# Optimization experiments

Hardware: AMD Instinct MI355X
Metric: run time of the kernel (lower is better)

Reference implementation:

```python
import jax, jax.numpy as jnp
import numpy as np

B, N, PAST = 2, 1024, 1024
DIM, HEADS, DH = 2048, 16, 128
INNER = HEADS * DH
LN_EPS = 1e-5
ROPE_THETA = 10000.0


def setup_inputs() -> dict:
    key = jax.random.key(0)
    k0, k1, k2, k3, k4 = jax.random.split(key, 5)
    x = jax.random.normal(k0, (B, N, DIM), dtype=jnp.float32)
    past_k = jax.random.normal(k1, (B, HEADS, PAST, DH), dtype=jnp.float32)
    past_v = jax.random.normal(k2, (B, HEADS, PAST, DH), dtype=jnp.float32)
    # causal mask with KV-cache offset: query i sits at global pos PAST+i,
    # mask (True = blocked) keys at positions j > PAST+i
    kv = PAST + N
    q_pos = PAST + jnp.arange(N)
    k_pos = jnp.arange(kv)
    mask = jnp.broadcast_to((k_pos[None, :] > q_pos[:, None])[None, None], (B, 1, N, kv))
    w_qkv = jax.random.normal(k3, (DIM, 3 * INNER), dtype=jnp.float32) * (DIM ** -0.5)
    w_out = jax.random.normal(k4, (INNER, DIM), dtype=jnp.float32) * (INNER ** -0.5)
    ln_g = jnp.ones((DIM,), dtype=jnp.float32)
    ln_b = jnp.zeros((DIM,), dtype=jnp.float32)
    return {"x": x, "past_k": past_k, "past_v": past_v, "mask": mask,
            "w_qkv": w_qkv, "w_out": w_out, "ln_g": ln_g, "ln_b": ln_b}


def _layernorm(x, g, b):
    mu = jnp.mean(x, axis=-1, keepdims=True)
    var = jnp.mean((x - mu) ** 2, axis=-1, keepdims=True)
    return (x - mu) * jax.lax.rsqrt(var + LN_EPS) * g + b


def _rope(t, pos):
    # interleaved rotary (lucidrains rotary-embedding-torch convention)
    inv_freq = 1.0 / (ROPE_THETA ** (jnp.arange(0, DH, 2, dtype=jnp.float32) / DH))
    freqs = pos.astype(jnp.float32)[:, None] * inv_freq[None, :]   # [n, DH/2]
    freqs = jnp.repeat(freqs, 2, axis=-1)                          # [n, DH]
    cos = jnp.cos(freqs).astype(t.dtype)
    sin = jnp.sin(freqs).astype(t.dtype)
    t2 = t.reshape(*t.shape[:-1], DH // 2, 2)
    rot = jnp.stack((-t2[..., 1], t2[..., 0]), axis=-1).reshape(t.shape)
    return t * cos + rot * sin


def reference(x, past_k, past_v, mask, w_qkv, w_out, ln_g, ln_b):
    b, n, _ = x.shape
    xn = _layernorm(x, ln_g, ln_b)
    qkv = xn @ w_qkv                                               # [b, n, 3*INNER]
    q, k, v = jnp.split(qkv, 3, axis=-1)
    to_heads = lambda t: t.reshape(b, n, HEADS, DH).transpose(0, 2, 1, 3)  # b h n d
    q, k, v = to_heads(q), to_heads(k), to_heads(v)
    k = jnp.concatenate((past_k, k), axis=2)                       # [b, h, kv, d]
    v = jnp.concatenate((past_v, v), axis=2)
    kv_len = k.shape[2]
    q = _rope(q, jnp.arange(n) + (kv_len - n))
    k = _rope(k, jnp.arange(kv_len))
    scale = DH ** -0.5
    dots = jnp.einsum('bhnd,bhmd->bhnm', q, k) * scale             # [b, h, n, kv]
    dots = jnp.where(mask, -jnp.inf, dots)
    attn = jax.nn.softmax(dots, axis=-1)
    out = jnp.einsum('bhnm,bhmd->bhnd', attn, v)                   # [b, h, n, d]
    out = out.transpose(0, 2, 1, 3).reshape(b, n, INNER)
    return out @ w_out, k, v
```

## Files before the change

kernel.cpp:

```cpp
#include <hip/hip_runtime.h>
#include <hip/hip_bf16.h>
#include <math.h>

#define BB    2
#define NN    1024
#define PAST  1024
#define KVL   2048
#define DIM   2048
#define HEADS 16
#define DH    128
#define INNER 2048
#define NQKV  6144
#define TOK   2048
#define LN_EPS 1e-5f

typedef __attribute__((ext_vector_type(8))) short   short8;
typedef __attribute__((ext_vector_type(4))) float   f32x4;
typedef __attribute__((ext_vector_type(8))) unsigned short us8;
typedef __attribute__((ext_vector_type(4))) unsigned short us4;
typedef unsigned short us;

__device__ __forceinline__ float bfbits2f(us u) {
    return __uint_as_float(((unsigned int)u) << 16);
}
__device__ __forceinline__ us f2bfb(float f) {
    union { __hip_bfloat16 h; us u; } cv;
    cv.h = __float2bfloat16(f);
    return cv.u;
}
__device__ __forceinline__ us8 pack8u(float4 a, float4 b) {
    us8 r;
    r[0] = f2bfb(a.x); r[1] = f2bfb(a.y); r[2] = f2bfb(a.z); r[3] = f2bfb(a.w);
    r[4] = f2bfb(b.x); r[5] = f2bfb(b.y); r[6] = f2bfb(b.z); r[7] = f2bfb(b.w);
    return r;
}

__device__ __forceinline__ void gload_lds16(const void* gsrc, void* ldst) {
    __builtin_amdgcn_global_load_lds(
        (const __attribute__((address_space(1))) void*)gsrc,
        (__attribute__((address_space(3))) void*)ldst, 16, 0, 0);
}

__global__ __launch_bounds__(256) void transp_kernel(
    const float* __restrict__ src, us* __restrict__ dst, int R, int C)
{
    const int c0 = blockIdx.x * 64;
    const int r0 = blockIdx.y * 64;
    const int tid = threadIdx.x;

    __shared__ us T[64][68];

    #pragma unroll
    for (int e = 0; e < 4; e++) {
        int idx = tid + e * 256;
        int jr  = idx >> 4;
        int c4  = (idx & 15) * 4;
        float4 v = *reinterpret_cast<const float4*>(
            src + (size_t)(r0 + jr) * C + c0 + c4);
        us4 w;
        w[0] = f2bfb(v.x); w[1] = f2bfb(v.y); w[2] = f2bfb(v.z); w[3] = f2bfb(v.w);
        *reinterpret_cast<us4*>(&T[jr][c4]) = w;
    }
    __syncthreads();

    #pragma unroll
    for (int e = 0; e < 4; e++) {
        int idx = tid + e * 256;
        int d   = idx >> 4;
        int k4  = (idx & 15) * 4;
        us4 w;
        w[0] = T[k4 + 0][d];
        w[1] = T[k4 + 1][d];
        w[2] = T[k4 + 2][d];
        w[3] = T[k4 + 3][d];
        *reinterpret_cast<us4*>(dst + (size_t)(c0 + d) * R + r0 + k4) = w;
    }
}

__global__ __launch_bounds__(256) void ln_kernel(
    const float* __restrict__ x, const float* __restrict__ g,
    const float* __restrict__ b, us* __restrict__ xn)
{
    const int t   = blockIdx.x;
    const int tid = threadIdx.x;
    const size_t base = (size_t)t * DIM;

    float4 p0 = reinterpret_cast<const float4*>(x + base)[tid * 2 + 0];
    float4 p1 = reinterpret_cast<const float4*>(x + base)[tid * 2 + 1];
    float v[8] = {p0.x, p0.y, p0.z, p0.w, p1.x, p1.y, p1.z, p1.w};

    float s1 = 0.f, s2 = 0.f;
    #pragma unroll
    for (int i = 0; i < 8; i++) { s1 += v[i]; s2 += v[i] * v[i]; }

    #pragma unroll
    for (int off = 32; off; off >>= 1) {
        s1 += __shfl_xor(s1, off);
        s2 += __shfl_xor(s2, off);
    }
    __shared__ float red1[4], red2[4];
    if ((tid & 63) == 0) { red1[tid >> 6] = s1; red2[tid >> 6] = s2; }
    __syncthreads();
    float S1 = red1[0] + red1[1] + red1[2] + red1[3];
    float S2 = red2[0] + red2[1] + red2[2] + red2[3];
    const float inv = 1.0f / (float)DIM;
    float mu  = S1 * inv;
    float var = S2 * inv - mu * mu;
    float rstd = rsqrtf(var + LN_EPS);

    const int d0 = tid * 8;
    float4 oa, ob;
    oa.x = (v[0] - mu) * rstd * g[d0 + 0] + b[d0 + 0];
    oa.y = (v[1] - mu) * rstd * g[d0 + 1] + b[d0 + 1];
    oa.z = (v[2] - mu) * rstd * g[d0 + 2] + b[d0 + 2];
    oa.w = (v[3] - mu) * rstd * g[d0 + 3] + b[d0 + 3];
    ob.x = (v[4] - mu) * rstd * g[d0 + 4] + b[d0 + 4];
    ob.y = (v[5] - mu) * rstd * g[d0 + 5] + b[d0 + 5];
    ob.z = (v[6] - mu) * rstd * g[d0 + 6] + b[d0 + 6];
    ob.w = (v[7] - mu) * rstd * g[d0 + 7] + b[d0 + 7];

    *reinterpret_cast<us8*>(xn + base + d0) = pack8u(oa, ob);
}

template<bool OUT_BF16>
__global__ __launch_bounds__(256) void gemm_bt_kernel(
    const us* __restrict__ A, const us* __restrict__ Bt,
    void* __restrict__ Cout, int M, int N, int K)
{
    __shared__ us As[2][128 * 32];
    __shared__ us Bs[2][128 * 32];

    const int tid  = threadIdx.x;
    const int wave = tid >> 6, lane = tid & 63;
    const int quad = lane >> 4, l16 = lane & 15;
    const int wm = wave & 1, wn = wave >> 1;
    const int m0 = blockIdx.y * 128, n0 = blockIdx.x * 128;

    f32x4 acc[4][4];
    #pragma unroll
    for (int i = 0; i < 4; i++)
        #pragma unroll
        for (int j = 0; j < 4; j++)
            #pragma unroll
            for (int r = 0; r < 4; r++) acc[i][j][r] = 0.f;

    const int s_row = tid >> 2;
    const int s_c8  = (tid & 3) * 8;

    auto stage = [&](int k0, int buf) {
        #pragma unroll
        for (int e = 0; e < 2; e++) {
            gload_lds16(A  + (size_t)(m0 + e * 64 + s_row) * K + k0 + s_c8,
                        (char*)&As[buf][0] + (e * 256 + tid) * 16);
            gload_lds16(Bt + (size_t)(n0 + e * 64 + s_row) * K + k0 + s_c8,
                        (char*)&Bs[buf][0] + (e * 256 + tid) * 16);
        }
    };

    stage(0, 0);
    __syncthreads();

    int buf = 0;
    for (int k0 = 0; k0 < K; k0 += 32) {
        if (k0 + 32 < K) stage(k0 + 32, buf ^ 1);

        short8 af[4], bf[4];
        #pragma unroll
        for (int mi = 0; mi < 4; mi++)
            af[mi] = *reinterpret_cast<const short8*>(
                &As[buf][(wm * 64 + mi * 16 + l16) * 32 + quad * 8]);
        #pragma unroll
        for (int ni = 0; ni < 4; ni++)
            bf[ni] = *reinterpret_cast<const short8*>(
                &Bs[buf][(wn * 64 + ni * 16 + l16) * 32 + quad * 8]);

        __builtin_amdgcn_s_setprio(1);
        #pragma unroll
        for (int mi = 0; mi < 4; mi++)
            #pragma unroll
            for (int ni = 0; ni < 4; ni++)
                acc[mi][ni] = __builtin_amdgcn_mfma_f32_16x16x32_bf16(
                    af[mi], bf[ni], acc[mi][ni], 0, 0, 0);
        __builtin_amdgcn_s_setprio(0);

        __syncthreads();
        buf ^= 1;
    }

    #pragma unroll
    for (int mi = 0; mi < 4; mi++) {
        #pragma unroll
        for (int r = 0; r < 4; r++) {
            size_t row = (size_t)(m0 + wm * 64 + mi * 16 + quad * 4 + r);
            #pragma unroll
            for (int ni = 0; ni < 4; ni++) {
                size_t col = n0 + wn * 64 + ni * 16 + l16;
                if (OUT_BF16)
                    ((us*)Cout)[row * N + col] = f2bfb(acc[mi][ni][r]);
                else
                    ((float*)Cout)[row * N + col] = acc[mi][ni][r];
            }
        }
    }
}

__global__ __launch_bounds__(256) void rope_kernel(
    const float* __restrict__ past_k, const float* __restrict__ past_v,
    us* __restrict__ qkv, float* __restrict__ out_k, float* __restrict__ out_v,
    us* __restrict__ Kbf)
{
    const int tid  = threadIdx.x;
    const int pid  = blockIdx.x * 4 + (tid >> 6);
    const int lane = tid & 63;

    const int b   = pid / (HEADS * KVL);
    const int rem = pid - b * (HEADS * KVL);
    const int h   = rem / KVL;
    const int pos = rem - h * KVL;

    const float invf = exp2f((float)lane * (-13.287712379549449f / 64.0f));
    float sn, cs;
    sincosf((float)pos * invf, &sn, &cs);

    const size_t obase = ((size_t)(b * HEADS + h) * KVL + pos) * DH + 2 * lane;

    float k0, k1;
    if (pos < PAST) {
        const size_t pbase = ((size_t)(b * HEADS + h) * PAST + pos) * DH + 2 * lane;
        k0 = past_k[pbase];
        k1 = past_k[pbase + 1];
    } else {
        const int t = b * NN + (pos - PAST);
        const us* qp = qkv + (size_t)t * NQKV + INNER + h * DH + 2 * lane;
        k0 = bfbits2f(qp[0]); k1 = bfbits2f(qp[1]);
    }
    float kr0 = k0 * cs - k1 * sn;
    float kr1 = k1 * cs + k0 * sn;
    out_k[obase]     = kr0;
    out_k[obase + 1] = kr1;
    Kbf[obase]       = f2bfb(kr0);
    Kbf[obase + 1]   = f2bfb(kr1);

    if (pos < PAST) {
        const size_t pbase = ((size_t)(b * HEADS + h) * PAST + pos) * DH + 2 * lane;
        out_v[obase]     = past_v[pbase];
        out_v[obase + 1] = past_v[pbase + 1];
    } else {
        const int t = b * NN + (pos - PAST);
        const us* vp = qkv + (size_t)t * NQKV + 2 * INNER + h * DH + 2 * lane;
        out_v[obase]     = bfbits2f(vp[0]);
        out_v[obase + 1] = bfbits2f(vp[1]);
    }

    if (pos >= PAST) {
        const int t = b * NN + (pos - PAST);
        us* qq = qkv + (size_t)t * NQKV + h * DH + 2 * lane;
        float q0 = bfbits2f(qq[0]), q1 = bfbits2f(qq[1]);
        qq[0] = f2bfb(q0 * cs - q1 * sn);
        qq[1] = f2bfb(q1 * cs + q0 * sn);
    }
}

__global__ __launch_bounds__(256) void vtrans_kernel(
    const float* __restrict__ Vc, us* __restrict__ Vtg)
{
    const int jb = blockIdx.x;
    const int db = blockIdx.y;
    const int bh = blockIdx.z;
    const int tid = threadIdx.x;

    __shared__ us T[64][68];

    const float* src = Vc + ((size_t)bh * KVL + jb * 64) * DH + db * 64;
    #pragma unroll
    for (int e = 0; e < 4; e++) {
        int idx = tid + e * 256;
        int jr  = idx >> 4;
        int c4  = (idx & 15) * 4;
        float4 v = *reinterpret_cast<const float4*>(src + (size_t)jr * DH + c4);
        us4 w;
        w[0] = f2bfb(v.x); w[1] = f2bfb(v.y); w[2] = f2bfb(v.z); w[3] = f2bfb(v.w);
        *reinterpret_cast<us4*>(&T[jr][c4]) = w;
    }
    __syncthreads();

    us* dst = Vtg + ((size_t)bh * DH + db * 64) * KVL + jb * 64;
    #pragma unroll
    for (int e = 0; e < 4; e++) {
        int idx = tid + e * 256;
        int d   = idx >> 4;
        int k4  = (idx & 15) * 4;
        us4 w;
        w[0] = T[k4 + 0][d];
        w[1] = T[k4 + 1][d];
        w[2] = T[k4 + 2][d];
        w[3] = T[k4 + 3][d];
        *reinterpret_cast<us4*>(dst + (size_t)d * KVL + k4) = w;
    }
}

__global__ __launch_bounds__(256) void attn_mfma_kernel(
    const us* __restrict__ qkv,
    const us* __restrict__ Kbf,
    const us* __restrict__ Vtg,
    us* __restrict__ Ao)
{
    const int qt   = blockIdx.x;
    const int h    = blockIdx.y;
    const int b    = blockIdx.z;
    const int tid  = threadIdx.x;
    const int wave = tid >> 6;
    const int lane = tid & 63;
    const int quad = lane >> 4;
    const int l16  = lane & 15;

    __shared__ us Ks[2][64 * 128];
    __shared__ us Vt[2][128 * 64];
    __shared__ us Pb[64][72];
    __shared__ float alF[4][16];

    short8 qf[4];
    {
        const int qrow = qt * 64 + wave * 16 + l16;
        const us* qp = qkv + (size_t)(b * NN + qrow) * NQKV + h * DH;
        #pragma unroll
        for (int ks = 0; ks < 4; ks++)
            qf[ks] = *reinterpret_cast<const short8*>(qp + ks * 32 + quad * 8);
    }

    f32x4 Oacc[8];
    #pragma unroll
    for (int t = 0; t < 8; t++)
        #pragma unroll
        for (int r = 0; r < 4; r++) Oacc[t][r] = 0.f;
    float m_run  = -INFINITY;
    float l_part = 0.f;

    const us* kptr = Kbf + (size_t)(b * HEADS + h) * KVL * DH;
    const us* vtb  = Vtg + (size_t)(b * HEADS + h) * DH * KVL;
    const float scale = 0.08838834764831845f;
    const float THRU  = 90.50966799f;
    const int qg  = PAST + qt * 64 + wave * 16 + l16;
    const int nch = 17 + qt;

    auto stage = [&](int j0, int buf) {
        #pragma unroll
        for (int e = 0; e < 4; e++) {
            int phys = (e * 256 + tid) * 16;
            int row  = phys >> 8;
            int col  = (phys & 255) ^ ((row & 7) << 4);
            gload_lds16((const char*)(kptr + (size_t)(j0 + row) * DH) + col,
                        (char*)&Ks[buf][0] + phys);
        }
        #pragma unroll
        for (int e = 0; e < 4; e++) {
            int phys = (e * 256 + tid) * 16;
            int row  = phys >> 7;
            int col  = (phys & 127) ^ ((row & 7) << 4);
            gload_lds16((const char*)(vtb + (size_t)row * KVL + j0) + col,
                        (char*)&Vt[buf][0] + phys);
        }
    };

    stage(0, 0);
    __syncthreads();

    int cur = 0;
    for (int c = 0; c < nch; c++) {
        const int j0 = c * 64;
        if (c + 1 < nch) stage(j0 + 64, cur ^ 1);

        f32x4 S[4];
        #pragma unroll
        for (int t = 0; t < 4; t++)
            #pragma unroll
            for (int r = 0; r < 4; r++) S[t][r] = 0.f;
        __builtin_amdgcn_s_setprio(1);
        #pragma unroll
        for (int ks = 0; ks < 4; ks++) {
            #pragma unroll
            for (int t = 0; t < 4; t++) {
                int row  = t * 16 + l16;
                int colb = ks * 64 + quad * 16;
                const char* p = (const char*)&Ks[cur][0] +
                                row * 256 + (colb ^ ((row & 7) << 4));
                short8 kb = *reinterpret_cast<const short8*>(p);
                S[t] = __builtin_amdgcn_mfma_f32_16x16x32_bf16(kb, qf[ks], S[t], 0, 0, 0);
            }
        }
        __builtin_amdgcn_s_setprio(0);

        const int rel = qg - j0;
        float mx = -INFINITY;
        #pragma unroll
        for (int t = 0; t < 4; t++) {
            #pragma unroll
            for (int r = 0; r < 4; r++) {
                int koff = t * 16 + quad * 4 + r;
                S[t][r] = (koff <= rel) ? S[t][r] : -INFINITY;
                mx = fmaxf(mx, S[t][r]);
            }
        }
        mx = fmaxf(mx, __shfl_xor(mx, 16));
        mx = fmaxf(mx, __shfl_xor(mx, 32));

        float alpha = 1.f;
        if (__any(mx > m_run + THRU)) {
            float nm = fmaxf(m_run, mx);
            alpha = __expf((m_run - nm) * scale);
            m_run = nm;
            if (quad == 0) alF[wave][l16] = alpha;
            asm volatile("s_waitcnt lgkmcnt(0)" ::: "memory");
            float a0 = alF[wave][quad * 4 + 0];
            float a1 = alF[wave][quad * 4 + 1];
            float a2 = alF[wave][quad * 4 + 2];
            float a3 = alF[wave][quad * 4 + 3];
            #pragma unroll
            for (int t2 = 0; t2 < 8; t2++) {
                Oacc[t2][0] *= a0; Oacc[t2][1] *= a1;
                Oacc[t2][2] *= a2; Oacc[t2][3] *= a3;
            }
        }

        const float nmk = -m_run * scale;
        float rs = 0.f;
        #pragma unroll
        for (int t = 0; t < 4; t++) {
            us4 w;
            #pragma unroll
            for (int r = 0; r < 4; r++) {
                float p = __expf(fmaf(S[t][r], scale, nmk));
                rs += p;
                w[r] = f2bfb(p);
            }
            *reinterpret_cast<us4*>(&Pb[wave * 16 + l16][t * 16 + quad * 4]) = w;
        }
        l_part = l_part * alpha + rs;

        asm volatile("s_waitcnt lgkmcnt(0)" ::: "memory");
        __builtin_amdgcn_sched_barrier(0);

        __builtin_amdgcn_s_setprio(1);
        #pragma unroll
        for (int kh = 0; kh < 2; kh++) {
            short8 pa = *reinterpret_cast<const short8*>(
                &Pb[wave * 16 + l16][kh * 32 + quad * 8]);
            #pragma unroll
            for (int t2 = 0; t2 < 8; t2++) {
                int row  = t2 * 16 + l16;
                int colb = kh * 64 + quad * 16;
                const char* p = (const char*)&Vt[cur][0] +
                                row * 128 + (colb ^ ((row & 7) << 4));
                short8 vb = *reinterpret_cast<const short8*>(p);
                Oacc[t2] = __builtin_amdgcn_mfma_f32_16x16x32_bf16(pa, vb, Oacc[t2], 0, 0, 0);
            }
        }
        __builtin_amdgcn_s_setprio(0);

        __syncthreads();
        cur ^= 1;
    }

    l_part += __shfl_xor(l_part, 16);
    l_part += __shfl_xor(l_part, 32);
    float invl[4];
    #pragma unroll
    for (int r = 0; r < 4; r++)
        invl[r] = 1.f / __shfl(l_part, quad * 4 + r);

    const int row0 = b * NN + qt * 64 + wave * 16 + quad * 4;
    #pragma unroll
    for (int r = 0; r < 4; r++) {
        us* dst = Ao + (size_t)(row0 + r) * INNER + h * DH + l16;
        #pragma unroll
        for (int t2 = 0; t2 < 8; t2++)
            dst[t2 * 16] = f2bfb(Oacc[t2][r] * invl[r]);
    }
}

extern "C" void kernel_launch(void* const* d_in, const int* in_sizes, int n_in,
                              void* d_out, int out_size, void* d_ws, size_t ws_size,
                              hipStream_t stream)
{
    const float* x      = (const float*)d_in[0];
    const float* past_k = (const float*)d_in[1];
    const float* past_v = (const float*)d_in[2];
    const float* w_qkv  = (const float*)d_in[4];
    const float* w_out  = (const float*)d_in[5];
    const float* ln_g   = (const float*)d_in[6];
    const float* ln_b   = (const float*)d_in[7];

    float* out   = (float*)d_out;
    float* out_k = out   + (size_t)BB * NN * DIM;
    float* out_v = out_k + (size_t)BB * HEADS * KVL * DH;

    us* xn   = (us*)d_ws;
    us* qkv  = xn  + (size_t)TOK * DIM;
    us* Wqt  = qkv + (size_t)TOK * NQKV;
    us* Wot  = Wqt + (size_t)NQKV * DIM;
    us* Vtg  = Wot + (size_t)DIM * INNER;
    us* attn = xn;
    us* Kbf  = Wqt;

    transp_kernel<<<dim3(NQKV / 64, DIM / 64), 256, 0, stream>>>(
        w_qkv, Wqt, DIM, NQKV);
    transp_kernel<<<dim3(DIM / 64, INNER / 64), 256, 0, stream>>>(
        w_out, Wot, INNER, DIM);

    ln_kernel<<<TOK, 256, 0, stream>>>(x, ln_g, ln_b, xn);

    gemm_bt_kernel<true><<<dim3(NQKV / 128, TOK / 128), 256, 0, stream>>>(
        xn, Wqt, (void*)qkv, TOK, NQKV, DIM);

    rope_kernel<<<(BB * HEADS * KVL) / 4, 256, 0, stream>>>(
        past_k, past_v, qkv, out_k, out_v, Kbf);

    vtrans_kernel<<<dim3(KVL / 64, DH / 64, BB * HEADS), 256, 0, stream>>>(
        out_v, Vtg);

    attn_mfma_kernel<<<dim3(NN / 64, HEADS, BB), 256, 0, stream>>>(
        qkv, Kbf, Vtg, attn);

    gemm_bt_kernel<false><<<dim3(DIM / 128, TOK / 128), 256, 0, stream>>>(
        attn, Wot, (void*)out, TOK, DIM, INNER);
}
```

Before: 381.3 us.

## Pair complementary causal query tiles per 512-thread attention block to balance work

The attention kernel now launches 256 blocks of 512 threads. Each block pairs query tile p with tile 15-p, so both halves share the same K/V staging and every block does a near-equal number of chunks, which removes the causal load imbalance. The flat block index is remapped so that neighbouring blocks cover different heads and batches. Alpha broadcast now uses shuffles instead of an LDS round-trip, and the per-wave P buffer is XOR-swizzled. The risk is idle waves in the low tile during the extra chunks, and lower occupancy from the larger blocks.

Measured after the change: 378.7 us. No clear change (-0.7%).

```diff
diff --git a/kernel.cpp b/kernel.cpp
--- a/kernel.cpp
+++ b/kernel.cpp
@@ -299,29 +299,35 @@
     }
 }
 
-__global__ __launch_bounds__(256) void attn_mfma_kernel(
+__global__ __launch_bounds__(512) void attn_mfma_kernel(
     const us* __restrict__ qkv,
     const us* __restrict__ Kbf,
     const us* __restrict__ Vtg,
     us* __restrict__ Ao)
 {
-    const int qt   = blockIdx.x;
-    const int h    = blockIdx.y;
-    const int b    = blockIdx.z;
     const int tid  = threadIdx.x;
     const int wave = tid >> 6;
     const int lane = tid & 63;
     const int quad = lane >> 4;
     const int l16  = lane & 15;
 
+    const int flat = blockIdx.x;
+    const int s    = flat >> 3;
+    const int g    = (flat & 7) + 8 * (s & 3);
+    const int p    = s >> 2;
+    const int h    = g & 15;
+    const int b    = g >> 4;
+    const int qtile = (wave < 4) ? p : (15 - p);
+    const int nch   = 32 - p;
+    const int mynch = (wave < 4) ? (17 + p) : (32 - p);
+
     __shared__ us Ks[2][64 * 128];
     __shared__ us Vt[2][128 * 64];
-    __shared__ us Pb[64][72];
-    __shared__ float alF[4][16];
+    __shared__ us Pb[8][16 * 64];
 
     short8 qf[4];
     {
-        const int qrow = qt * 64 + wave * 16 + l16;
+        const int qrow = qtile * 64 + (wave & 3) * 16 + l16;
         const us* qp = qkv + (size_t)(b * NN + qrow) * NQKV + h * DH;
         #pragma unroll
         for (int ks = 0; ks < 4; ks++)
@@ -340,24 +346,25 @@
     const us* vtb  = Vtg + (size_t)(b * HEADS + h) * DH * KVL;
     const float scale = 0.08838834764831845f;
     const float THRU  = 90.50966799f;
-    const int qg  = PAST + qt * 64 + wave * 16 + l16;
-    const int nch = 17 + qt;
+    const int qg  = PAST + qtile * 64 + (wave & 3) * 16 + l16;
+    const int swz = (l16 & 7) << 4;
+    char* pbb = (char*)&Pb[wave][0];
 
     auto stage = [&](int j0, int buf) {
         #pragma unroll
-        for (int e = 0; e < 4; e++) {
-            int phys = (e * 256 + tid) * 16;
+        for (int e = 0; e < 2; e++) {
+            int phys = (e * 512 + tid) * 16;
             int row  = phys >> 8;
             int col  = (phys & 255) ^ ((row & 7) << 4);
             gload_lds16((const char*)(kptr + (size_t)(j0 + row) * DH) + col,
                         (char*)&Ks[buf][0] + phys);
         }
         #pragma unroll
-        for (int e = 0; e < 4; e++) {
-            int phys = (e * 256 + tid) * 16;
+        for (int e = 0; e < 2; e++) {
+            int phys = (e * 512 + tid) * 16;
             int row  = phys >> 7;
             int col  = (phys & 127) ^ ((row & 7) << 4);
-            gload_lds16((const char*)(vtb + (size_t)row * KVL + j0) + col,
+            gload_lds16((const char*)(vtb + (size_t)row * KVL) + j0 * 2 + col,
                         (char*)&Vt[buf][0] + phys);
         }
     };
@@ -370,92 +377,92 @@
         const int j0 = c * 64;
         if (c + 1 < nch) stage(j0 + 64, cur ^ 1);
 
-        f32x4 S[4];
-        #pragma unroll
-        for (int t = 0; t < 4; t++)
-            #pragma unroll
-            for (int r = 0; r < 4; r++) S[t][r] = 0.f;
-        __builtin_amdgcn_s_setprio(1);
-        #pragma unroll
-        for (int ks = 0; ks < 4; ks++) {
+        if (c < mynch) {
+            f32x4 S[4];
+            #pragma unroll
+            for (int t = 0; t < 4; t++)
+                #pragma unroll
+                for (int r = 0; r < 4; r++) S[t][r] = 0.f;
+            __builtin_amdgcn_s_setprio(1);
+            #pragma unroll
+            for (int ks = 0; ks < 4; ks++) {
+                #pragma unroll
+                for (int t = 0; t < 4; t++) {
+                    int row  = t * 16 + l16;
+                    int colb = ks * 64 + quad * 16;
+                    const char* kp = (const char*)&Ks[cur][0] +
+                                    row * 256 + (colb ^ ((row & 7) << 4));
+                    short8 kb = *reinterpret_cast<const short8*>(kp);
+                    S[t] = __builtin_amdgcn_mfma_f32_16x16x32_bf16(kb, qf[ks], S[t], 0, 0, 0);
+                }
+            }
+            __builtin_amdgcn_s_setprio(0);
+
+            const int rel = qg - j0;
+            float mx = -INFINITY;
             #pragma unroll
             for (int t = 0; t < 4; t++) {
-                int row  = t * 16 + l16;
-                int colb = ks * 64 + quad * 16;
-                const char* p = (const char*)&Ks[cur][0] +
-                                row * 256 + (colb ^ ((row & 7) << 4));
-                short8 kb = *reinterpret_cast<const short8*>(p);
-                S[t] = __builtin_amdgcn_mfma_f32_16x16x32_bf16(kb, qf[ks], S[t], 0, 0, 0);
+                #pragma unroll
+                for (int r = 0; r < 4; r++) {
+                    int koff = t * 16 + quad * 4 + r;
+                    S[t][r] = (koff <= rel) ? S[t][r] : -INFINITY;
+                    mx = fmaxf(mx, S[t][r]);
+                }
             }
+            mx = fmaxf(mx, __shfl_xor(mx, 16));
+            mx = fmaxf(mx, __shfl_xor(mx, 32));
+
+            float alpha = 1.f;
+            if (__any(mx > m_run + THRU)) {
+                float nm = fmaxf(m_run, mx);
+                alpha = __expf((m_run - nm) * scale);
+                m_run = nm;
+                float al[4];
+                #pragma unroll
+                for (int r = 0; r < 4; r++) al[r] = __shfl(alpha, quad * 4 + r);
+                #pragma unroll
+                for (int t2 = 0; t2 < 8; t2++) {
+                    Oacc[t2][0] *= al[0]; Oacc[t2][1] *= al[1];
+                    Oacc[t2][2] *= al[2]; Oacc[t2][3] *= al[3];
+                }
+            }
+
+            const float nmk = -m_run * scale;
+            float rs = 0.f;
+            #pragma unroll
+            for (int t = 0; t < 4; t++) {
+                us4 w;
+                #pragma unroll
+                for (int r = 0; r < 4; r++) {
+                    float pv = __expf(fmaf(S[t][r], scale, nmk));
+                    rs += pv;
+                    w[r] = f2bfb(pv);
+                }
+                *reinterpret_cast<us4*>(pbb + l16 * 128 +
+                                        ((t * 32 + quad * 8) ^ swz)) = w;
+            }
+            l_part = l_part * alpha + rs;
+
+            asm volatile("s_waitcnt lgkmcnt(0)" ::: "memory");
+            __builtin_amdgcn_sched_barrier(0);
+
+            __builtin_amdgcn_s_setprio(1);
+            #pragma unroll
+            for (int kh = 0; kh < 2; kh++) {
+                short8 pa = *reinterpret_cast<const short8*>(
+                    pbb + l16 * 128 + ((kh * 64 + quad * 16) ^ swz));
+                #pragma unroll
+                for (int t2 = 0; t2 < 8; t2++) {
+                    int row  = t2 * 16 + l16;
+                    int colb = kh * 64 + quad * 16;
+                    const char* vp = (const char*)&Vt[cur][0] +
+                                    row * 128 + (colb ^ ((row & 7) << 4));
+                    short8 vb = *reinterpret_cast<const short8*>(vp);
+                    Oacc[t2] = __builtin_amdgcn_mfma_f32_16x16x32_bf16(pa, vb, Oacc[t2], 0, 0, 0);
+                }
+            }
+            __builtin_amdgcn_s_setprio(0);
         }
-        __builtin_amdgcn_s_setprio(0);
-
-        const int rel = qg - j0;
-        float mx = -INFINITY;
-        #pragma unroll
-        for (int t = 0; t < 4; t++) {
-            #pragma unroll
-            for (int r = 0; r < 4; r++) {
-                int koff = t * 16 + quad * 4 + r;
-                S[t][r] = (koff <= rel) ? S[t][r] : -INFINITY;
-                mx = fmaxf(mx, S[t][r]);
-            }
-        }
-        mx = fmaxf(mx, __shfl_xor(mx, 16));
-        mx = fmaxf(mx, __shfl_xor(mx, 32));
-
-        float alpha = 1.f;
-        if (__any(mx > m_run + THRU)) {
-            float nm = fmaxf(m_run, mx);
-            alpha = __expf((m_run - nm) * scale);
-            m_run = nm;
-            if (quad == 0) alF[wave][l16] = alpha;
-            asm volatile("s_waitcnt lgkmcnt(0)" ::: "memory");
-            float a0 = alF[wave][quad * 4 + 0];
-            float a1 = alF[wave][quad * 4 + 1];
-            float a2 = alF[wave][quad * 4 + 2];
-            float a3 = alF[wave][quad * 4 + 3];
-            #pragma unroll
-            for (int t2 = 0; t2 < 8; t2++) {
-                Oacc[t2][0] *= a0; Oacc[t2][1] *= a1;
-                Oacc[t2][2] *= a2; Oacc[t2][3] *= a3;
-            }
-        }
-
-        const float nmk = -m_run * scale;
-        float rs = 0.f;
-        #pragma unroll
-        for (int t = 0; t < 4; t++) {
-            us4 w;
-            #pragma unroll
-            for (int r = 0; r < 4; r++) {
-                float p = __expf(fmaf(S[t][r], scale, nmk));
-                rs += p;
-                w[r] = f2bfb(p);
-            }
-            *reinterpret_cast<us4*>(&Pb[wave * 16 + l16][t * 16 + quad * 4]) = w;
-        }
-        l_part = l_part * alpha + rs;
-
-        asm volatile("s_waitcnt lgkmcnt(0)" ::: "memory");
-        __builtin_amdgcn_sched_barrier(0);
-
-        __builtin_amdgcn_s_setprio(1);
-        #pragma unroll
-        for (int kh = 0; kh < 2; kh++) {
-            short8 pa = *reinterpret_cast<const short8*>(
-                &Pb[wave * 16 + l16][kh * 32 + quad * 8]);
-            #pragma unroll
-            for (int t2 = 0; t2 < 8; t2++) {
-                int row  = t2 * 16 + l16;
-                int colb = kh * 64 + quad * 16;
-                const char* p = (const char*)&Vt[cur][0] +
-                                row * 128 + (colb ^ ((row & 7) << 4));
-                short8 vb = *reinterpret_cast<const short8*>(p);
-                Oacc[t2] = __builtin_amdgcn_mfma_f32_16x16x32_bf16(pa, vb, Oacc[t2], 0, 0, 0);
-            }
-        }
-        __builtin_amdgcn_s_setprio(0);
 
         __syncthreads();
         cur ^= 1;
@@ -468,7 +475,7 @@
     for (int r = 0; r < 4; r++)
         invl[r] = 1.f / __shfl(l_part, quad * 4 + r);
 
-    const int row0 = b * NN + qt * 64 + wave * 16 + quad * 4;
+    const int row0 = b * NN + qtile * 64 + (wave & 3) * 16 + quad * 4;
     #pragma unroll
     for (int r = 0; r < 4; r++) {
         us* dst = Ao + (size_t)(row0 + r) * INNER + h * DH + l16;
@@ -518,7 +525,7 @@
     vtrans_kernel<<<dim3(KVL / 64, DH / 64, BB * HEADS), 256, 0, stream>>>(
         out_v, Vtg);
 
-    attn_mfma_kernel<<<dim3(NN / 64, HEADS, BB), 256, 0, stream>>>(
+    attn_mfma_kernel<<<256, 512, 0, stream>>>(
         qkv, Kbf, Vtg, attn);
 
     gemm_bt_kernel<false><<<dim3(DIM / 128, TOK / 128), 256, 0, stream>>>(
```
